# Performance work log

Measured on AMD Instinct MI355X. Metric: run time of the kernel, lower is better.

Reference implementation:

```python
import jax, jax.numpy as jnp
import numpy as np

D_MODEL = 1024
NUM_HEADS = 16
DEPTH = D_MODEL // NUM_HEADS
BATCH = 2
SEQ = 2048


def setup_inputs() -> dict:
    key = jax.random.key(0)
    ks = jax.random.split(key, 12)
    s = 1.0 / np.sqrt(D_MODEL)
    inp = {
        'v': jax.random.normal(ks[0], (BATCH, SEQ, D_MODEL), jnp.float32),
        'k': jax.random.normal(ks[1], (BATCH, SEQ, D_MODEL), jnp.float32),
        'q': jax.random.normal(ks[2], (BATCH, SEQ, D_MODEL), jnp.float32),
        # causal mask: 1.0 where attention is disallowed (strict upper triangle)
        'mask': jnp.triu(jnp.ones((1, 1, SEQ, SEQ), jnp.float32), k=1),
        'Wq': jax.random.normal(ks[3], (D_MODEL, D_MODEL), jnp.float32) * s,
        'bq': jnp.zeros((D_MODEL,), jnp.float32),
        'Wk': jax.random.normal(ks[4], (D_MODEL, D_MODEL), jnp.float32) * s,
        'bk': jnp.zeros((D_MODEL,), jnp.float32),
        'Wv': jax.random.normal(ks[5], (D_MODEL, D_MODEL), jnp.float32) * s,
        'bv': jnp.zeros((D_MODEL,), jnp.float32),
        'Wo': jax.random.normal(ks[6], (D_MODEL, D_MODEL), jnp.float32) * s,
        'bo': jnp.zeros((D_MODEL,), jnp.float32),
    }
    return inp


def _split_heads(x):
    b, s, _ = x.shape
    return x.reshape(b, s, NUM_HEADS, DEPTH).transpose(0, 2, 1, 3)  # [B,H,S,Dh]


def reference(v, k, q, mask, Wq, bq, Wk, bk, Wv, bv, Wo, bo):
    b = q.shape[0]
    qh = _split_heads(q @ Wq.T + bq)
    kh = _split_heads(k @ Wk.T + bk)
    vh = _split_heads(v @ Wv.T + bv)
    scores = jnp.einsum('bhsd,bhtd->bhst', qh, kh) / jnp.sqrt(
        jnp.asarray(DEPTH, jnp.float32))
    scores = scores + mask * (-1e9)
    attn = jax.nn.softmax(scores, axis=-1)
    out = jnp.einsum('bhst,bhtd->bhsd', attn, vh)
    out = out.transpose(0, 2, 1, 3).reshape(b, -1, D_MODEL)
    return out @ Wo.T + bo
```

## Files before the change

kernel.cpp:

```cpp
#include <hip/hip_runtime.h>
#include <hip/hip_bf16.h>

#define D_MODEL 1024
#define NHEADS 16
#define DEPTH 64
#define BATCH 2
#define SEQ 2048
#define NTOK (BATCH * SEQ)

#define QSCALE 0.180336884f
#define DEFER_THR 11.5415603f

typedef short bf16x8 __attribute__((ext_vector_type(8)));
typedef float f32x4 __attribute__((ext_vector_type(4)));
typedef float f32x16 __attribute__((ext_vector_type(16)));
typedef unsigned short ushortx8 __attribute__((ext_vector_type(8)));
typedef unsigned uint2v __attribute__((ext_vector_type(2)));

using gas_ptr = const __attribute__((address_space(1))) unsigned int*;
using las_ptr = __attribute__((address_space(3))) unsigned int*;

__device__ __forceinline__ unsigned short f2bf(float f) {
    union { float f; unsigned u; } v; v.f = f;
    unsigned r = v.u + 0x7fffu + ((v.u >> 16) & 1u);
    return (unsigned short)(r >> 16);
}

__device__ __forceinline__ unsigned cvtpk(float lo, float hi) {
    unsigned r;
    asm("v_cvt_pk_bf16_f32 %0, %1, %2" : "=v"(r) : "v"(lo), "v"(hi));
    return r;
}

__device__ __forceinline__ uint2v pls(unsigned a, unsigned b) {
    return __builtin_amdgcn_permlane32_swap(a, b, false, false);
}

__device__ __forceinline__ void gload16(const void* g, void* l) {
    __builtin_amdgcn_global_load_lds((gas_ptr)g, (las_ptr)l, 16, 0, 0);
}

__global__ __launch_bounds__(256) void convert_bf16(
    const float* __restrict__ q, const float* __restrict__ k, const float* __restrict__ v,
    const float* __restrict__ wq, const float* __restrict__ wk,
    const float* __restrict__ wv, const float* __restrict__ wo,
    unsigned short* __restrict__ qb, unsigned short* __restrict__ kb,
    unsigned short* __restrict__ vb,
    unsigned short* __restrict__ wqb, unsigned short* __restrict__ wkb,
    unsigned short* __restrict__ wvb, unsigned short* __restrict__ wob)
{
    const int ACT = (NTOK * D_MODEL) / 8;
    const int WT  = (D_MODEL * D_MODEL) / 8;
    const int total = 3 * ACT + 4 * WT;
    for (int i = blockIdx.x * 256 + threadIdx.x; i < total; i += gridDim.x * 256) {
        const float* s; unsigned short* d; int off; float sc = 1.f;
        if (i < ACT)            { s = q; d = qb; off = i; }
        else if (i < 2 * ACT)   { s = k; d = kb; off = i - ACT; }
        else if (i < 3 * ACT)   { s = v; d = vb; off = i - 2 * ACT; }
        else {
            int j = i - 3 * ACT;
            int wsel = j >> 17;  off = j & (WT - 1);
            s = (wsel == 0) ? wq : (wsel == 1) ? wk : (wsel == 2) ? wv : wo;
            d = (wsel == 0) ? wqb : (wsel == 1) ? wkb : (wsel == 2) ? wvb : wob;
            if (wsel == 0) sc = QSCALE;
        }
        float4 a = ((const float4*)s)[off * 2];
        float4 b = ((const float4*)s)[off * 2 + 1];
        ushortx8 r;
        r[0] = f2bf(a.x * sc); r[1] = f2bf(a.y * sc);
        r[2] = f2bf(a.z * sc); r[3] = f2bf(a.w * sc);
        r[4] = f2bf(b.x * sc); r[5] = f2bf(b.y * sc);
        r[6] = f2bf(b.z * sc); r[7] = f2bf(b.w * sc);
        ((ushortx8*)d)[off] = r;
    }
}

template<int IT, int DEST, bool QKV>
__global__ __launch_bounds__(256) void gemm_bf16(
    const unsigned short* __restrict__ A0, const unsigned short* __restrict__ A1,
    const unsigned short* __restrict__ A2,
    const unsigned short* __restrict__ B0, const unsigned short* __restrict__ B1,
    const unsigned short* __restrict__ B2,
    const float* __restrict__ bias0, const float* __restrict__ bias1,
    const float* __restrict__ bias2,
    void* __restrict__ C0, void* __restrict__ C1, void* __restrict__ C2,
    int M, int N, int K)
{
    constexpr int BM = IT * 32;
    constexpr int WROWS = IT * 16;
    __shared__ unsigned short As[2][BM * 32];
    __shared__ unsigned short Bs[2][128 * 32];

    const unsigned short* A = A0; const unsigned short* Bw = B0;
    const float* bias = bias0;    void* Cp = C0;
    float bsc = 1.f;
    int zz = 0;
    if (QKV) {
        zz = blockIdx.z;
        if (zz == 0) bsc = QSCALE;
        if (zz == 1) { A = A1; Bw = B1; bias = bias1; Cp = C1; }
        else if (zz == 2) { A = A2; Bw = B2; bias = bias2; Cp = C2; }
    }

    const int tid  = threadIdx.x;
    const int lane = tid & 63;
    const int w    = tid >> 6;
    const int wu   = __builtin_amdgcn_readfirstlane(w);
    const int wr   = w >> 1, wc = w & 1;
    const int lr   = lane & 15, lg = lane >> 4;

    const int row0 = blockIdx.x * BM;
    const int n0   = blockIdx.y * 128;

    const int cA0 = wu * 64 + lane;
    const unsigned short* gA0 = A + (size_t)(row0 + (cA0 >> 2)) * K + (cA0 & 3) * 8;
    const unsigned short* gA1 = nullptr;
    if (IT == 4) {
        const int cA1 = 256 + cA0;
        gA1 = A + (size_t)(row0 + (cA1 >> 2)) * K + (cA1 & 3) * 8;
    }
    const unsigned short* gB0 = Bw + (size_t)(n0 + (cA0 >> 2)) * K + (cA0 & 3) * 8;
    const unsigned short* gB1;
    {
        const int cB1 = 256 + cA0;
        gB1 = Bw + (size_t)(n0 + (cB1 >> 2)) * K + (cB1 & 3) * 8;
    }

    auto STAGE = [&](int kt, int buf) {
        gload16(gA0 + kt, &As[buf][wu * 512]);
        if (IT == 4) gload16(gA1 + kt, &As[buf][2048 + wu * 512]);
        gload16(gB0 + kt, &Bs[buf][wu * 512]);
        gload16(gB1 + kt, &Bs[buf][2048 + wu * 512]);
    };

    f32x4 acc[IT][4];
    for (int i = 0; i < IT; ++i)
        for (int j = 0; j < 4; ++j)
            for (int r = 0; r < 4; ++r) acc[i][j][r] = 0.f;

    STAGE(0, 0);
    __syncthreads();

    const int NT = K / 32;
    int cur = 0;
    for (int t = 0; t < NT; ++t) {
        if (t + 1 < NT) STAGE((t + 1) * 32, cur ^ 1);

        bf16x8 af[IT], bfr[4];
#pragma unroll
        for (int i = 0; i < IT; ++i)
            af[i] = *(const bf16x8*)&As[cur][(wr * WROWS + i * 16 + lr) * 32 + lg * 8];
#pragma unroll
        for (int j = 0; j < 4; ++j)
            bfr[j] = *(const bf16x8*)&Bs[cur][(wc * 64 + j * 16 + lr) * 32 + lg * 8];
#pragma unroll
        for (int i = 0; i < IT; ++i)
#pragma unroll
            for (int j = 0; j < 4; ++j)
                acc[i][j] = __builtin_amdgcn_mfma_f32_16x16x32_bf16(
                    af[i], bfr[j], acc[i][j], 0, 0, 0);

        __syncthreads();
        cur ^= 1;
    }

    for (int i = 0; i < IT; ++i) {
        for (int j = 0; j < 4; ++j) {
            int gcol = n0 + wc * 64 + j * 16 + lr;
            float bv = bias[gcol] * bsc;
            int s0full = row0 + wr * WROWS + i * 16 + lg * 4;
            if (QKV && zz == 1) {
                int b_ = s0full >> 11, sr = s0full & (SEQ - 1);
                int h_ = gcol >> 6, dh = gcol & 63;
                int jt_ = sr >> 6, t0 = sr & 63;
                int tb_ = t0 >> 5, m0 = t0 & 31;
                int dk_ = dh >> 4, hi_ = (dh >> 3) & 1, e_ = dh & 7;
                unsigned short* Kf = (unsigned short*)Cp;
                size_t base = ((size_t)(b_ * NHEADS + h_) * (SEQ >> 6) + jt_) * 4096
                            + (size_t)((tb_ * 4 + dk_) * 64 + hi_ * 32) * 8 + e_;
#pragma unroll
                for (int r = 0; r < 4; ++r)
                    Kf[base + (size_t)(m0 + r) * 8] = f2bf(acc[i][j][r] + bv);
            } else if (QKV && zz == 2) {
                int b_ = s0full >> 11, sr = s0full & (SEQ - 1);
                int h_ = gcol >> 6, dh = gcol & 63;
                int jt_ = sr >> 6, t0 = sr & 63;
                int ts_ = t0 >> 4, hi_ = (t0 >> 3) & 1, e0 = t0 & 7;
                int dblk = dh >> 5, m_ = dh & 31;
                unsigned w0 = (unsigned)f2bf(acc[i][j][0] + bv)
                            | ((unsigned)f2bf(acc[i][j][1] + bv) << 16);
                unsigned w1 = (unsigned)f2bf(acc[i][j][2] + bv)
                            | ((unsigned)f2bf(acc[i][j][3] + bv) << 16);
                unsigned long long pk = (unsigned long long)w0
                                      | ((unsigned long long)w1 << 32);
                unsigned short* Vf = (unsigned short*)Cp;
                size_t idx = ((size_t)(b_ * NHEADS + h_) * (SEQ >> 6) + jt_) * 4096
                           + (size_t)((dblk * 4 + ts_) * 64 + hi_ * 32 + m_) * 8 + e0;
                *(unsigned long long*)&Vf[idx] = pk;
            } else if (DEST == 0) {
#pragma unroll
                for (int r = 0; r < 4; ++r) {
                    int grow = s0full + r;
                    float val = acc[i][j][r] + bv;
                    int b_ = grow >> 11, s = grow & (SEQ - 1);
                    int h_ = gcol >> 6, dh = gcol & 63;
                    ((unsigned short*)Cp)[(((size_t)b_ * NHEADS + h_) * SEQ + s) * DEPTH + dh]
                        = f2bf(val);
                }
            } else {
#pragma unroll
                for (int r = 0; r < 4; ++r) {
                    int grow = s0full + r;
                    ((float*)Cp)[(size_t)grow * N + gcol] = acc[i][j][r] + bv;
                }
            }
        }
    }
}

#define KLOAD(JT, KF)                                                          \
{                                                                              \
    const unsigned short* Kt_ = Kb + (size_t)(JT) * 4096;                      \
    _Pragma("unroll")                                                          \
    for (int f_ = 0; f_ < 8; ++f_)                                             \
        KF[f_] = *(const bf16x8*)&Kt_[(size_t)f_ * 512 + lane * 8];            \
}

#define TILE_BODY(KC, KN)                                                      \
{                                                                              \
    const unsigned short* Vg = Vb + (size_t)jt * 4096;                         \
    bf16x8 vf0[4], vf1[4];                                                     \
    _Pragma("unroll")                                                          \
    for (int ts = 0; ts < 4; ++ts) {                                           \
        vf0[ts] = *(const bf16x8*)&Vg[(size_t)ts * 512 + lane * 8];            \
        vf1[ts] = *(const bf16x8*)&Vg[(size_t)(4 + ts) * 512 + lane * 8];      \
    }                                                                          \
    if (jt + 2 < ntiles) { KLOAD(jt + 2, KN) }                                 \
    f32x16 st[2];                                                              \
    __builtin_amdgcn_s_setprio(1);                                             \
    _Pragma("unroll")                                                          \
    for (int tb = 0; tb < 2; ++tb) {                                           \
        f32x16 a;                                                              \
        _Pragma("unroll") for (int r = 0; r < 16; ++r) a[r] = 0.f;             \
        _Pragma("unroll")                                                      \
        for (int dk = 0; dk < 4; ++dk)                                         \
            a = __builtin_amdgcn_mfma_f32_32x32x16_bf16(KC[tb * 4 + dk], qf[dk], a, 0, 0, 0); \
        st[tb] = a;                                                            \
    }                                                                          \
    __builtin_amdgcn_s_setprio(0);                                             \
    if (jt == ntiles - 1) {                                                    \
        _Pragma("unroll")                                                      \
        for (int tb = 0; tb < 2; ++tb)                                         \
            _Pragma("unroll")                                                  \
            for (int r = 0; r < 16; ++r) {                                     \
                int t = jt * 64 + tb * 32 + (r & 3) + 8 * (r >> 2) + 4 * hi;   \
                if (t > qr0 + m) st[tb][r] = -1e9f;                            \
            }                                                                  \
    }                                                                          \
    float tmx[16];                                                             \
    _Pragma("unroll")                                                          \
    for (int r = 0; r < 16; ++r) tmx[r] = fmaxf(st[0][r], st[1][r]);           \
    _Pragma("unroll")                                                          \
    for (int sft = 8; sft; sft >>= 1)                                          \
        _Pragma("unroll")                                                      \
        for (int r = 0; r < 8; ++r)                                            \
            if (r < sft) tmx[r] = fmaxf(tmx[r], tmx[r + sft]);                 \
    float tmax;                                                                \
    {                                                                          \
        union { float f; unsigned u; } cu_; cu_.f = tmx[0];                    \
        uint2v rr_ = pls(cu_.u, cu_.u);                                        \
        union { unsigned u; float f; } a_, b_; a_.u = rr_[0]; b_.u = rr_[1];   \
        tmax = fmaxf(a_.f, b_.f);                                              \
    }                                                                          \
    if (!__all(tmax <= mrun + DEFER_THR)) {                                    \
        float mnew = fmaxf(mrun, tmax);                                        \
        float sc = exp2f(mrun - mnew);                                         \
        mrun = mnew; lrun *= sc;                                               \
        if (hi == 0) scbw[m] = sc;                                             \
        f32x4 s4[4];                                                           \
        _Pragma("unroll")                                                      \
        for (int g = 0; g < 4; ++g) s4[g] = *(f32x4*)&scbw[g * 8 + hi * 4];    \
        _Pragma("unroll")                                                      \
        for (int r = 0; r < 16; ++r) {                                         \
            float f = s4[r >> 2][r & 3];                                       \
            o0[r] *= f; o1[r] *= f;                                            \
        }                                                                      \
    }                                                                          \
    float psum = 0.f;                                                          \
    _Pragma("unroll")                                                          \
    for (int tb = 0; tb < 2; ++tb)                                             \
        _Pragma("unroll")                                                      \
        for (int r = 0; r < 16; ++r) {                                         \
            float p = exp2f(st[tb][r] - mrun);                                 \
            st[tb][r] = p; psum += p;                                          \
        }                                                                      \
    {                                                                          \
        union { float f; unsigned u; } cu_; cu_.f = psum;                      \
        uint2v rr_ = pls(cu_.u, cu_.u);                                        \
        union { unsigned u; float f; } a_, b_; a_.u = rr_[0]; b_.u = rr_[1];   \
        lrun += a_.f + b_.f;                                                   \
    }                                                                          \
    unsigned pkw[8][2];                                                        \
    _Pragma("unroll")                                                          \
    for (int G = 0; G < 8; ++G) {                                              \
        const int tb = G >> 2, g = G & 3;                                      \
        pkw[G][0] = cvtpk(st[tb][4 * g + 0], st[tb][4 * g + 1]);               \
        pkw[G][1] = cvtpk(st[tb][4 * g + 2], st[tb][4 * g + 3]);               \
    }                                                                          \
    __builtin_amdgcn_s_setprio(1);                                             \
    _Pragma("unroll")                                                          \
    for (int ts = 0; ts < 4; ++ts) {                                           \
        uint2v s0_ = pls(pkw[2 * ts][0], pkw[2 * ts + 1][0]);                  \
        uint2v s1_ = pls(pkw[2 * ts][1], pkw[2 * ts + 1][1]);                  \
        union { unsigned u[4]; bf16x8 v; } uu;                                 \
        uu.u[0] = s0_[0]; uu.u[1] = s1_[0]; uu.u[2] = s0_[1]; uu.u[3] = s1_[1]; \
        o0 = __builtin_amdgcn_mfma_f32_32x32x16_bf16(uu.v, vf0[ts], o0, 0, 0, 0); \
        o1 = __builtin_amdgcn_mfma_f32_32x32x16_bf16(uu.v, vf1[ts], o1, 0, 0, 0); \
    }                                                                          \
    __builtin_amdgcn_s_setprio(0);                                             \
}

__global__ __launch_bounds__(128, 2) void attn_wave(
    const unsigned short* __restrict__ Qh, const unsigned short* __restrict__ Kh,
    const unsigned short* __restrict__ Vt, unsigned short* __restrict__ ctx)
{
    __shared__ __align__(16) float scb[2][32];
    __shared__ __align__(16) float mlbuf[2][2][32];
    __shared__ __align__(16) float c0b[32], c1b[32], invb[32];
    __shared__ __align__(16) float osh0[16][64], osh1[16][64];

    const int tid  = threadIdx.x;
    const int ww   = tid >> 6;
    const int lane = tid & 63;
    const int m    = lane & 31;
    const int hi   = lane >> 5;
    float* scbw = scb[ww];

    const int bid  = blockIdx.x;
    const int bh   = bid & 31;
    const int qb   = 63 - (bid >> 5);
    const int qr0  = qb * 32;

    const int b = bh >> 4, h = bh & 15;
    const unsigned short* Qb = Qh + ((size_t)bh * SEQ + qr0) * DEPTH;
    const unsigned short* Kb = Kh + (size_t)bh * SEQ * DEPTH;
    const unsigned short* Vb = Vt + (size_t)bh * SEQ * DEPTH;

    bf16x8 qf[4];
#pragma unroll
    for (int dk = 0; dk < 4; ++dk)
        qf[dk] = *(const bf16x8*)&Qb[(size_t)m * DEPTH + dk * 16 + hi * 8];

    f32x16 o0, o1;
#pragma unroll
    for (int r = 0; r < 16; ++r) { o0[r] = 0.f; o1[r] = 0.f; }
    float mrun = -1e30f, lrun = 0.f;

    const int ntiles = (qb >> 1) + 1;
    bf16x8 kfA[8], kfB[8];

    int jt = ww;
    if (jt < ntiles) {
        KLOAD(jt, kfA)
        while (true) {
            TILE_BODY(kfA, kfB)
            jt += 2; if (jt >= ntiles) break;
            TILE_BODY(kfB, kfA)
            jt += 2; if (jt >= ntiles) break;
        }
    }

    if (hi == 0) { mlbuf[ww][0][m] = mrun; mlbuf[ww][1][m] = lrun; }
    __syncthreads();
    if (ww == 0 && hi == 0) {
        float m0 = mlbuf[0][0][m], l0 = mlbuf[0][1][m];
        float m1 = mlbuf[1][0][m], l1 = mlbuf[1][1][m];
        float M  = fmaxf(m0, m1);
        float c0 = exp2f(m0 - M), c1 = exp2f(m1 - M);
        c0b[m] = c0; c1b[m] = c1;
        invb[m] = 1.0f / (l0 * c0 + l1 * c1);
    }
    __syncthreads();

    const float* cb = (ww == 0) ? c0b : c1b;
    f32x4 fc[4];
#pragma unroll
    for (int g = 0; g < 4; ++g)
        fc[g] = *(const f32x4*)&cb[g * 8 + hi * 4];
#pragma unroll
    for (int r = 0; r < 16; ++r) {
        float f = fc[r >> 2][r & 3];
        o0[r] *= f; o1[r] *= f;
    }
    if (ww == 0) {
#pragma unroll
        for (int r = 0; r < 16; ++r) { osh0[r][lane] = o0[r]; osh1[r][lane] = o1[r]; }
    }
    __syncthreads();
    if (ww == 1) {
        f32x4 fi[4];
#pragma unroll
        for (int g = 0; g < 4; ++g)
            fi[g] = *(const f32x4*)&invb[g * 8 + hi * 4];
#pragma unroll
        for (int r = 0; r < 16; ++r) {
            float inv = fi[r >> 2][r & 3];
            int ml = (r & 3) + 8 * (r >> 2) + 4 * hi;
            size_t rowbase = ((size_t)b * SEQ + qr0 + ml) * D_MODEL + h * DEPTH;
            ctx[rowbase + m]      = f2bf((o0[r] + osh0[r][lane]) * inv);
            ctx[rowbase + 32 + m] = f2bf((o1[r] + osh1[r][lane]) * inv);
        }
    }
}

extern "C" void kernel_launch(void* const* d_in, const int* in_sizes, int n_in,
                              void* d_out, int out_size, void* d_ws, size_t ws_size,
                              hipStream_t stream) {
    const float* v  = (const float*)d_in[0];
    const float* k  = (const float*)d_in[1];
    const float* q  = (const float*)d_in[2];
    const float* Wq = (const float*)d_in[4];
    const float* bq = (const float*)d_in[5];
    const float* Wk = (const float*)d_in[6];
    const float* bk = (const float*)d_in[7];
    const float* Wv = (const float*)d_in[8];
    const float* bv = (const float*)d_in[9];
    const float* Wo = (const float*)d_in[10];
    const float* bo = (const float*)d_in[11];

    char* ws = (char*)d_ws;
    const size_t MB = 1024 * 1024;
    unsigned short* Qb  = (unsigned short*)(ws + 0);
    unsigned short* Kb  = (unsigned short*)(ws + 8  * MB);
    unsigned short* Vb  = (unsigned short*)(ws + 16 * MB);
    unsigned short* Wqb = (unsigned short*)(ws + 24 * MB);
    unsigned short* Wkb = (unsigned short*)(ws + 26 * MB);
    unsigned short* Wvb = (unsigned short*)(ws + 28 * MB);
    unsigned short* Wob = (unsigned short*)(ws + 30 * MB);
    unsigned short* Qh  = (unsigned short*)(ws + 32 * MB);
    unsigned short* Kh  = (unsigned short*)(ws + 40 * MB);
    unsigned short* Vtt = (unsigned short*)(ws + 48 * MB);
    unsigned short* ctx = Qb;

    convert_bf16<<<2048, 256, 0, stream>>>(q, k, v, Wq, Wk, Wv, Wo,
                                           Qb, Kb, Vb, Wqb, Wkb, Wvb, Wob);

    gemm_bf16<4, 0, true><<<dim3(32, 8, 3), 256, 0, stream>>>(
        Qb, Kb, Vb, Wqb, Wkb, Wvb, bq, bk, bv,
        (void*)Qh, (void*)Kh, (void*)Vtt, NTOK, D_MODEL, D_MODEL);

    attn_wave<<<dim3(2048), 128, 0, stream>>>(Qh, Kh, Vtt, ctx);

    gemm_bf16<2, 1, false><<<dim3(64, 8), 256, 0, stream>>>(
        ctx, nullptr, nullptr, Wob, nullptr, nullptr, bo, nullptr, nullptr,
        d_out, nullptr, nullptr, NTOK, D_MODEL, D_MODEL);
}
```

Measured before the change: 116.3 us.

## Triple-buffer GEMM LDS staging with vmcnt waits and tree-reduce softmax row sums

The bf16 GEMM moves from a double-buffered LDS pipeline with two __syncthreads per k-step to a three-stage ring. It prefetches two tiles ahead, waits on the vector memory counter and uses a single barrier per iteration, so global loads overlap more of the MFMA work. Separately, the softmax row-sum in attention now uses a pairwise tree reduction instead of a serial accumulation chain, which shortens the dependency chain. The cost is 50% more LDS for staging, which may lower occupancy, and the hand-written vmcnt counts depend on the exact number of loads issued per stage.

```diff
diff --git a/kernel.cpp b/kernel.cpp
--- a/kernel.cpp
+++ b/kernel.cpp
@@ -88,8 +88,9 @@
 {
     constexpr int BM = IT * 32;
     constexpr int WROWS = IT * 16;
-    __shared__ unsigned short As[2][BM * 32];
-    __shared__ unsigned short Bs[2][128 * 32];
+    constexpr int ASZ = BM * 32;
+    __shared__ unsigned short As[3 * ASZ];
+    __shared__ unsigned short Bs[3 * 4096];
 
     const unsigned short* A = A0; const unsigned short* Bw = B0;
     const float* bias = bias0;    void* Cp = C0;
@@ -127,10 +128,10 @@
     }
 
     auto STAGE = [&](int kt, int buf) {
-        gload16(gA0 + kt, &As[buf][wu * 512]);
-        if (IT == 4) gload16(gA1 + kt, &As[buf][2048 + wu * 512]);
-        gload16(gB0 + kt, &Bs[buf][wu * 512]);
-        gload16(gB1 + kt, &Bs[buf][2048 + wu * 512]);
+        gload16(gA0 + kt, &As[buf * ASZ + wu * 512]);
+        if (IT == 4) gload16(gA1 + kt, &As[buf * ASZ + 2048 + wu * 512]);
+        gload16(gB0 + kt, &Bs[buf * 4096 + wu * 512]);
+        gload16(gB1 + kt, &Bs[buf * 4096 + 2048 + wu * 512]);
     };
 
     f32x4 acc[IT][4];
@@ -138,21 +139,36 @@
         for (int j = 0; j < 4; ++j)
             for (int r = 0; r < 4; ++r) acc[i][j][r] = 0.f;
 
+    const int NT = K / 32;
     STAGE(0, 0);
-    __syncthreads();
-
-    const int NT = K / 32;
+    STAGE(32, 1);
+
     int cur = 0;
     for (int t = 0; t < NT; ++t) {
-        if (t + 1 < NT) STAGE((t + 1) * 32, cur ^ 1);
+        if (t < NT - 1) {
+            if constexpr (IT == 4)
+                asm volatile("s_waitcnt vmcnt(4)" ::: "memory");
+            else
+                asm volatile("s_waitcnt vmcnt(3)" ::: "memory");
+        } else {
+            asm volatile("s_waitcnt vmcnt(0)" ::: "memory");
+        }
+        __builtin_amdgcn_s_barrier();
+        __builtin_amdgcn_sched_barrier(0);
 
         bf16x8 af[IT], bfr[4];
 #pragma unroll
         for (int i = 0; i < IT; ++i)
-            af[i] = *(const bf16x8*)&As[cur][(wr * WROWS + i * 16 + lr) * 32 + lg * 8];
+            af[i] = *(const bf16x8*)&As[cur * ASZ + (wr * WROWS + i * 16 + lr) * 32 + lg * 8];
 #pragma unroll
         for (int j = 0; j < 4; ++j)
-            bfr[j] = *(const bf16x8*)&Bs[cur][(wc * 64 + j * 16 + lr) * 32 + lg * 8];
+            bfr[j] = *(const bf16x8*)&Bs[cur * 4096 + (wc * 64 + j * 16 + lr) * 32 + lg * 8];
+
+        if (t + 2 < NT) {
+            int nb = cur + 2; if (nb >= 3) nb -= 3;
+            STAGE((t + 2) * 32, nb);
+        }
+
 #pragma unroll
         for (int i = 0; i < IT; ++i)
 #pragma unroll
@@ -160,8 +176,7 @@
                 acc[i][j] = __builtin_amdgcn_mfma_f32_16x16x32_bf16(
                     af[i], bfr[j], acc[i][j], 0, 0, 0);
 
-        __syncthreads();
-        cur ^= 1;
+        cur = (cur == 2) ? 0 : cur + 1;
     }
 
     for (int i = 0; i < IT; ++i) {
@@ -286,16 +301,21 @@
             o0[r] *= f; o1[r] *= f;                                            \
         }                                                                      \
     }                                                                          \
-    float psum = 0.f;                                                          \
     _Pragma("unroll")                                                          \
     for (int tb = 0; tb < 2; ++tb)                                             \
         _Pragma("unroll")                                                      \
-        for (int r = 0; r < 16; ++r) {                                         \
-            float p = exp2f(st[tb][r] - mrun);                                 \
-            st[tb][r] = p; psum += p;                                          \
-        }                                                                      \
+        for (int r = 0; r < 16; ++r)                                           \
+            st[tb][r] = exp2f(st[tb][r] - mrun);                               \
+    float s16[16];                                                             \
+    _Pragma("unroll")                                                          \
+    for (int r = 0; r < 16; ++r) s16[r] = st[0][r] + st[1][r];                 \
+    _Pragma("unroll")                                                          \
+    for (int sft = 8; sft; sft >>= 1)                                          \
+        _Pragma("unroll")                                                      \
+        for (int r = 0; r < 8; ++r)                                            \
+            if (r < sft) s16[r] += s16[r + sft];                               \
     {                                                                          \
-        union { float f; unsigned u; } cu_; cu_.f = psum;                      \
+        union { float f; unsigned u; } cu_; cu_.f = s16[0];                    \
         uint2v rr_ = pls(cu_.u, cu_.u);                                        \
         union { unsigned u; float f; } a_, b_; a_.u = rr_[0]; b_.u = rr_[1];   \
         lrun += a_.f + b_.f;                                                   \
```

After: 112.7 us, median of 3. 3.2% less time.
